# Optimization experiments

Measured on AMD Instinct MI355X. Metric: run time of the kernel, lower is better.

Reference implementation:

```python
import jax, jax.numpy as jnp
import numpy as np

N_NODES = 50000
N_EDGES = 800000
NFEAT = 96
NHID = 96
NCLASS = 40


def setup_inputs() -> dict:
    key = jax.random.key(0)
    ks = jax.random.split(key, 8)
    x = jax.random.normal(ks[0], (N_NODES, NFEAT), dtype=jnp.float32)
    edge_index = jax.random.randint(ks[1], (2, N_EDGES), 0, N_NODES, dtype=jnp.int64)
    def glorot(k, shape):
        fan_in = shape[1]
        bound = 1.0 / np.sqrt(fan_in)
        return jax.random.uniform(k, shape, jnp.float32, -bound, bound)
    return {
        'x': x,
        'edge_index': edge_index,
        'W1_l': glorot(ks[2], (NHID, NFEAT)),
        'b1_l': jnp.zeros((NHID,), jnp.float32),
        'W1_r': glorot(ks[3], (NHID, NFEAT)),
        'W2_l': glorot(ks[4], (NCLASS, NHID)),
        'b2_l': jnp.zeros((NCLASS,), jnp.float32),
        'W2_r': glorot(ks[5], (NCLASS, NHID)),
    }


def _sage_conv(x, src, dst, W_l, b_l, W_r):
    # gather neighbor features per edge, scatter-mean onto dst nodes
    msg = x[src]                                   # [E, F]
    agg = jax.ops.segment_sum(msg, dst, num_segments=N_NODES)   # [N, F]
    cnt = jax.ops.segment_sum(jnp.ones((src.shape[0],), x.dtype), dst,
                              num_segments=N_NODES)             # [N]
    agg = agg / jnp.maximum(cnt, 1.0)[:, None]
    # lin_l(agg) + lin_r(x)
    return agg @ W_l.T + b_l + x @ W_r.T


def reference(x, edge_index, W1_l, b1_l, W1_r, W2_l, b2_l, W2_r):
    src, dst = edge_index[0], edge_index[1]
    h = _sage_conv(x, src, dst, W1_l, b1_l, W1_r)
    h = jax.nn.relu(h)  # dropout is identity in eval mode
    h = _sage_conv(h, src, dst, W2_l, b2_l, W2_r)
    return jax.nn.log_softmax(h, axis=1)
```

## Files before the change

kernel.cpp:

```cpp
#include <hip/hip_runtime.h>
#include <math.h>

#define NCLASS 40
#define BSH    6
#define BSIZE  64
#define MAXB   1024
#define EPB    4096
#define LCOL   2048

typedef __attribute__((ext_vector_type(8))) short short8;
typedef __attribute__((ext_vector_type(4))) float float4v;

__device__ __forceinline__ unsigned short f2bf(float f) {
    union { float f; unsigned u; } v; v.f = f;
    unsigned r = v.u + 0x7fffu + ((v.u >> 16) & 1u);
    return (unsigned short)(r >> 16);
}
__device__ __forceinline__ float bf2f(unsigned int s) {
    union { unsigned u; float f; } v; v.u = s << 16; return v.f;
}

__global__ __launch_bounds__(256) void convhist_kernel(const int* __restrict__ ei,
                                                       const float4* __restrict__ x4,
                                                       const float* __restrict__ W1l,
                                                       const float* __restrict__ W1r,
                                                       const float* __restrict__ W2l,
                                                       const float* __restrict__ W2r,
                                                       int* __restrict__ histT,
                                                       unsigned short* __restrict__ axb,
                                                       unsigned short* __restrict__ wb1,
                                                       unsigned short* __restrict__ wb2,
                                                       int N, int E, int nbucket,
                                                       int nbin, int xblocks) {
    __shared__ int hcnt[MAXB];
    int tid = threadIdx.x;
    int blk = blockIdx.x;
    if (blk < nbin) {
        for (int t = tid; t < nbucket; t += 256) hcnt[t] = 0;
        __syncthreads();
        int e0 = blk * EPB;
        for (int it = 0; it < EPB / 256; ++it) {
            int e = e0 + it * 256 + tid;
            if (e < E) atomicAdd(&hcnt[ei[E + e] >> BSH], 1);
        }
        __syncthreads();
        for (int t = tid; t < nbucket; t += 256)
            histT[t * nbin + blk] = hcnt[t];
        return;
    }
    if (blk < nbin + xblocks) {
        int idx = (blk - nbin) * 256 + tid;
        if (idx >= N * 24) return;
        int n = idx / 24, q = idx - n * 24;
        float4 v = x4[idx];
        ushort4 o;
        o.x = f2bf(v.x); o.y = f2bf(v.y); o.z = f2bf(v.z); o.w = f2bf(v.w);
        *(ushort4*)(axb + (size_t)n * 192 + 96 + q * 4) = o;
        return;
    }
    int t = (blk - nbin - xblocks) * 256 + tid;
    const float* src;
    unsigned short* dst;
    if (t < 36 * 64) {
        int s = t >> 6, lane = t & 63;
        int kc = s / 6, jt = s - kc * 6;
        int j  = jt * 16 + (lane & 15);
        int k2 = kc * 32 + (lane >> 4) * 8;
        src = (k2 < 96) ? (W1l + j * 96 + k2) : (W1r + j * 96 + (k2 - 96));
        dst = wb1 + t * 8;
    } else if (t < 51 * 64) {
        int t2 = t - 36 * 64;
        int s = t2 >> 6, lane = t2 & 63;
        int kc = s / 5, jt = s - kc * 5;
        int j  = jt * 16 + (lane & 15);
        int k2 = kc * 32 + (lane >> 4) * 8;
        src = (j < 40) ? (W2l + j * 96 + k2) : (W2r + (j - 40) * 96 + k2);
        dst = wb2 + t2 * 8;
    } else return;
    ushort4 o0, o1;
    o0.x = f2bf(src[0]); o0.y = f2bf(src[1]); o0.z = f2bf(src[2]); o0.w = f2bf(src[3]);
    o1.x = f2bf(src[4]); o1.y = f2bf(src[5]); o1.z = f2bf(src[6]); o1.w = f2bf(src[7]);
    *(ushort4*)(dst)     = o0;
    *(ushort4*)(dst + 4) = o1;
}

__global__ __launch_bounds__(256) void bsum_kernel(int* __restrict__ histT,
                                                   int* __restrict__ gbh, int nbin) {
    __shared__ int s[256];
    int k = blockIdx.x, tid = threadIdx.x;
    int v = (tid < nbin) ? histT[k * nbin + tid] : 0;
    s[tid] = v;
    __syncthreads();
    for (int off = 1; off < 256; off <<= 1) {
        int o = (tid >= off) ? s[tid - off] : 0;
        __syncthreads();
        s[tid] += o;
        __syncthreads();
    }
    if (tid < nbin) histT[k * nbin + tid] = s[tid] - v;
    if (tid == 255) gbh[k] = s[255];
}

__global__ __launch_bounds__(256) void bscan_kernel(const int* __restrict__ gbh,
                                                    int* __restrict__ gbase,
                                                    int* __restrict__ rp,
                                                    int N, int E, int nbucket) {
    __shared__ int s[256];
    int tid  = threadIdx.x;
    int base = tid * 4;
    int w0 = (base     < nbucket) ? gbh[base]     : 0;
    int w1 = (base + 1 < nbucket) ? gbh[base + 1] : 0;
    int w2 = (base + 2 < nbucket) ? gbh[base + 2] : 0;
    int w3 = (base + 3 < nbucket) ? gbh[base + 3] : 0;
    int tsum = w0 + w1 + w2 + w3;
    s[tid] = tsum;
    __syncthreads();
    for (int off = 1; off < 256; off <<= 1) {
        int o = (tid >= off) ? s[tid - off] : 0;
        __syncthreads();
        s[tid] += o;
        __syncthreads();
    }
    int excl = s[tid] - tsum;
    if (base < nbucket) {
        gbase[base] = excl;
        if (base + 1 <= nbucket) gbase[base + 1] = excl + w0;
        if (base + 2 <= nbucket) gbase[base + 2] = excl + w0 + w1;
        if (base + 3 <= nbucket) gbase[base + 3] = excl + w0 + w1 + w2;
    }
    if (tid == 0) { gbase[nbucket] = E; rp[N] = E; }
}

__global__ __launch_bounds__(256) void bin_kernel(const int* __restrict__ ei,
                                                  const int* __restrict__ gbase,
                                                  const int* __restrict__ histT,
                                                  unsigned int* __restrict__ tmp,
                                                  int E, int nbucket, int nbin) {
    __shared__ int lcnt[MAXB];
    __shared__ int lbase[MAXB];
    int tid = threadIdx.x;
    for (int t = tid; t < nbucket; t += 256) {
        lbase[t] = gbase[t] + histT[t * nbin + blockIdx.x];
        lcnt[t]  = 0;
    }
    __syncthreads();
    int e0 = blockIdx.x * EPB;
    for (int it = 0; it < EPB / 256; ++it) {
        int e = e0 + it * 256 + tid;
        if (e < E) {
            int src = ei[e], dst = ei[E + e];
            int b   = dst >> BSH;
            int ofs = atomicAdd(&lcnt[b], 1);
            tmp[lbase[b] + ofs] = (unsigned)src | ((unsigned)(dst & (BSIZE - 1)) << 16);
        }
    }
}

__global__ __launch_bounds__(256) void csr_agg_kernel(const unsigned int* __restrict__ tmp,
                                                      const int* __restrict__ gbase,
                                                      int* __restrict__ rp,
                                                      unsigned short* __restrict__ col,
                                                      unsigned short* __restrict__ axb,
                                                      int N) {
    __shared__ int ncnt[BSIZE], nofs[BSIZE], sscan[BSIZE];
    __shared__ unsigned short lcol[LCOL];
    int b   = blockIdx.x;
    int tid = threadIdx.x;
    int s0 = gbase[b], s1 = gbase[b + 1];
    int cnt = s1 - s0;
    bool inl = (cnt <= LCOL);
    if (tid < BSIZE) ncnt[tid] = 0;
    __syncthreads();
    for (int i = s0 + tid; i < s1; i += 256)
        atomicAdd(&ncnt[tmp[i] >> 16], 1);
    __syncthreads();
    int v = (tid < BSIZE) ? ncnt[tid] : 0;
    if (tid < BSIZE) sscan[tid] = v;
    __syncthreads();
    for (int off = 1; off < BSIZE; off <<= 1) {
        int o = (tid < BSIZE && tid >= off) ? sscan[tid - off] : 0;
        __syncthreads();
        if (tid < BSIZE) sscan[tid] += o;
        __syncthreads();
    }
    if (tid < BSIZE) {
        nofs[tid] = sscan[tid] - v;
        int node = (b << BSH) + tid;
        if (node < N) rp[node] = s0 + nofs[tid];
        ncnt[tid] = 0;
    }
    __syncthreads();
    for (int i = s0 + tid; i < s1; i += 256) {
        unsigned int t2 = tmp[i];
        int d   = t2 >> 16;
        int ofs = atomicAdd(&ncnt[d], 1);
        int pos = nofs[d] + ofs;
        unsigned short sv = (unsigned short)(t2 & 0xffffu);
        col[s0 + pos] = sv;
        if (inl) lcol[pos] = sv;
    }
    __syncthreads();
    int nodebase = b << BSH;
    auto gather = [&](auto getc) {
        for (int item = tid; item < BSIZE * 12; item += 256) {
            int nl = item / 12;
            int q  = item - nl * 12;
            int ls  = nofs[nl];
            int deg = ncnt[nl];
            int le  = ls + deg;
            float a0=0.f,a1=0.f,a2=0.f,a3=0.f,a4=0.f,a5=0.f,a6=0.f,a7=0.f;
            int i = ls;
            for (; i + 7 < le; i += 8) {
                #pragma unroll
                for (int u = 0; u < 8; ++u) {
                    int c = getc(i + u);
                    uint4 w = *(const uint4*)(axb + (size_t)c * 192 + 96 + q * 8);
                    a0 += bf2f(w.x & 0xffffu); a1 += bf2f(w.x >> 16);
                    a2 += bf2f(w.y & 0xffffu); a3 += bf2f(w.y >> 16);
                    a4 += bf2f(w.z & 0xffffu); a5 += bf2f(w.z >> 16);
                    a6 += bf2f(w.w & 0xffffu); a7 += bf2f(w.w >> 16);
                }
            }
            for (; i < le; ++i) {
                int c = getc(i);
                uint4 w = *(const uint4*)(axb + (size_t)c * 192 + 96 + q * 8);
                a0 += bf2f(w.x & 0xffffu); a1 += bf2f(w.x >> 16);
                a2 += bf2f(w.y & 0xffffu); a3 += bf2f(w.y >> 16);
                a4 += bf2f(w.z & 0xffffu); a5 += bf2f(w.z >> 16);
                a6 += bf2f(w.w & 0xffffu); a7 += bf2f(w.w >> 16);
            }
            float inv = 1.0f / (float)(deg > 1 ? deg : 1);
            ushort4 o0, o1;
            o0.x = f2bf(a0 * inv); o0.y = f2bf(a1 * inv);
            o0.z = f2bf(a2 * inv); o0.w = f2bf(a3 * inv);
            o1.x = f2bf(a4 * inv); o1.y = f2bf(a5 * inv);
            o1.z = f2bf(a6 * inv); o1.w = f2bf(a7 * inv);
            *(ushort4*)(axb + (size_t)(nodebase + nl) * 192 + q * 8)     = o0;
            *(ushort4*)(axb + (size_t)(nodebase + nl) * 192 + q * 8 + 4) = o1;
        }
    };
    if (inl) gather([&](int i) { return (int)lcol[i]; });
    else     gather([&](int i) { return (int)col[s0 + i]; });
}

__global__ __launch_bounds__(256) void l1proj_kernel(const unsigned short* __restrict__ axb,
                                                     const unsigned short* __restrict__ wb1,
                                                     const float* __restrict__ b1,
                                                     const unsigned short* __restrict__ wb2,
                                                     const float* __restrict__ b2,
                                                     unsigned short* __restrict__ pl,
                                                     float* __restrict__ pr,
                                                     int N) {
    __shared__ unsigned short sh[128 * 104];
    int wave = threadIdx.x >> 6, lane = threadIdx.x & 63;
    int nbase = blockIdx.x * 128 + wave * 32;
    int lbase = wave * 32;
    int mrow = lane & 15, quad = lane >> 4;

    {
        float4v acc[2][6] = {};
        const short8* W = (const short8*)wb1;
        #pragma unroll
        for (int kc = 0; kc < 6; ++kc) {
            short8 a0 = *(const short8*)(axb + (size_t)(nbase + mrow)      * 192 + kc * 32 + quad * 8);
            short8 a1 = *(const short8*)(axb + (size_t)(nbase + 16 + mrow) * 192 + kc * 32 + quad * 8);
            #pragma unroll
            for (int jt = 0; jt < 6; ++jt) {
                short8 b = W[(kc * 6 + jt) * 64 + lane];
                acc[0][jt] = __builtin_amdgcn_mfma_f32_16x16x32_bf16(a0, b, acc[0][jt], 0, 0, 0);
                acc[1][jt] = __builtin_amdgcn_mfma_f32_16x16x32_bf16(a1, b, acc[1][jt], 0, 0, 0);
            }
        }
        #pragma unroll
        for (int jt = 0; jt < 6; ++jt) {
            int j = jt * 16 + mrow;
            float bj = b1[j];
            #pragma unroll
            for (int mt = 0; mt < 2; ++mt) {
                #pragma unroll
                for (int r = 0; r < 4; ++r) {
                    int nl = lbase + mt * 16 + quad * 4 + r;
                    sh[nl * 104 + j] = f2bf(fmaxf(acc[mt][jt][r] + bj, 0.f));
                }
            }
        }
    }
    __syncthreads();
    {
        float4v acc[2][5] = {};
        const short8* W = (const short8*)wb2;
        #pragma unroll
        for (int kc = 0; kc < 3; ++kc) {
            short8 a0 = *(const short8*)&sh[(lbase + mrow)      * 104 + kc * 32 + quad * 8];
            short8 a1 = *(const short8*)&sh[(lbase + 16 + mrow) * 104 + kc * 32 + quad * 8];
            #pragma unroll
            for (int jt = 0; jt < 5; ++jt) {
                short8 b = W[(kc * 5 + jt) * 64 + lane];
                acc[0][jt] = __builtin_amdgcn_mfma_f32_16x16x32_bf16(a0, b, acc[0][jt], 0, 0, 0);
                acc[1][jt] = __builtin_amdgcn_mfma_f32_16x16x32_bf16(a1, b, acc[1][jt], 0, 0, 0);
            }
        }
        #pragma unroll
        for (int jt = 0; jt < 5; ++jt) {
            int j = jt * 16 + mrow;
            float b2v = (j >= 40) ? b2[j - 40] : 0.f;
            #pragma unroll
            for (int mt = 0; mt < 2; ++mt) {
                #pragma unroll
                for (int r = 0; r < 4; ++r) {
                    int node = nbase + mt * 16 + quad * 4 + r;
                    if (node < N) {
                        float v = acc[mt][jt][r];
                        if (j < 40) pl[(size_t)node * 64 + j] = f2bf(v);
                        else        pr[(size_t)node * 40 + (j - 40)] = v + b2v;
                    }
                }
            }
        }
    }
}

__global__ __launch_bounds__(256) void final_kernel(const unsigned short* __restrict__ pl,
                                                    const float* __restrict__ pr,
                                                    const int* __restrict__ rp,
                                                    const unsigned short* __restrict__ col,
                                                    float* __restrict__ out, int N) {
    __shared__ float red[4][6][40];
    int wave = threadIdx.x >> 6;
    int lane = threadIdx.x & 63;
    int n = blockIdx.x * 4 + wave;
    if (n >= N) return;
    int s = rp[n], e = rp[n + 1];
    int g = lane / 10;
    int c = lane - g * 10;
    bool gok = (g < 6);
    float a0 = 0.f, a1 = 0.f, a2 = 0.f, a3 = 0.f;
    for (int base = s; base < e; base += 6) {
        int idx = base + g;
        if (gok && idx < e) {
            int cn = col[idx];
            uint2 u = *(const uint2*)(pl + (size_t)cn * 64 + c * 4);
            a0 += bf2f(u.x & 0xffffu); a1 += bf2f(u.x >> 16);
            a2 += bf2f(u.y & 0xffffu); a3 += bf2f(u.y >> 16);
        }
    }
    if (gok) {
        float4 t; t.x = a0; t.y = a1; t.z = a2; t.w = a3;
        *(float4*)&red[wave][g][c * 4] = t;
    }
    bool act = (lane < NCLASS);
    float v = -INFINITY;
    if (act) {
        float val = 0.f;
        #pragma unroll
        for (int gg = 0; gg < 6; ++gg) val += red[wave][gg][lane];
        int deg = e - s;
        float inv = 1.0f / (float)(deg > 1 ? deg : 1);
        v = val * inv + pr[(size_t)n * 40 + lane];
    }
    float m = v;
    #pragma unroll
    for (int off = 32; off >= 1; off >>= 1) m = fmaxf(m, __shfl_xor(m, off));
    float ex = act ? __expf(v - m) : 0.f;
    float ssum = ex;
    #pragma unroll
    for (int off = 32; off >= 1; off >>= 1) ssum += __shfl_xor(ssum, off);
    if (act) out[(size_t)n * 40 + lane] = v - m - __logf(ssum);
}

extern "C" void kernel_launch(void* const* d_in, const int* in_sizes, int n_in,
                              void* d_out, int out_size, void* d_ws, size_t ws_size,
                              hipStream_t stream) {
    const float* x   = (const float*)d_in[0];
    const int*   ei  = (const int*)  d_in[1];
    const float* W1l = (const float*)d_in[2];
    const float* b1  = (const float*)d_in[3];
    const float* W1r = (const float*)d_in[4];
    const float* W2l = (const float*)d_in[5];
    const float* b2  = (const float*)d_in[6];
    const float* W2r = (const float*)d_in[7];
    float* out = (float*)d_out;

    const int N = in_sizes[0] / 96;
    const int E = in_sizes[1] / 2;
    const int nbucket = (N + BSIZE - 1) >> BSH;
    const int nbin = (E + EPB - 1) / EPB;
    const int NB   = (N + 127) / 128;
    const int NP2  = NB * 128;
    const int xblocks = (N * 24 + 255) / 256;

    auto al = [](size_t v) { return (v + 255) & ~(size_t)255; };
    char* ws = (char*)d_ws;
    size_t o = 0;
    int* histT = (int*)(ws + o); o = al(o + (size_t)MAXB * 256 * 4);
    int* gbh   = (int*)(ws + o); o = al(o + (size_t)MAXB * 4);
    int* gbase = (int*)(ws + o); o = al(o + (size_t)(MAXB + 1) * 4);
    int* rp    = (int*)(ws + o); o = al(o + (size_t)(N + 1) * 4);
    unsigned int*   tmp = (unsigned int*)(ws + o);   o = al(o + (size_t)E * 4);
    unsigned short* col = (unsigned short*)(ws + o); o = al(o + (size_t)E * 2);
    unsigned short* axb = (unsigned short*)(ws + o); o = al(o + (size_t)NP2 * 192 * 2);
    unsigned short* wb1 = (unsigned short*)(ws + o); o = al(o + 36 * 64 * 8 * 2);
    unsigned short* wb2 = (unsigned short*)(ws + o); o = al(o + 15 * 64 * 8 * 2);
    unsigned short* pl  = (unsigned short*)(ws + o); o = al(o + (size_t)NP2 * 64 * 2);
    float*          pr  = (float*)(ws + o);          o = al(o + (size_t)N * 40 * 4);

    convhist_kernel<<<nbin + xblocks + 13, 256, 0, stream>>>(
        ei, (const float4*)x, W1l, W1r, W2l, W2r, histT, axb, wb1, wb2,
        N, E, nbucket, nbin, xblocks);
    bsum_kernel <<<nbucket, 256, 0, stream>>>(histT, gbh, nbin);
    bscan_kernel<<<1, 256, 0, stream>>>(gbh, gbase, rp, N, E, nbucket);
    bin_kernel  <<<nbin, 256, 0, stream>>>(ei, gbase, histT, tmp, E, nbucket, nbin);
    csr_agg_kernel<<<nbucket, 256, 0, stream>>>(tmp, gbase, rp, col, axb, N);
    l1proj_kernel<<<NB, 256, 0, stream>>>(axb, wb1, b1, wb2, b2, pl, pr, N);
    final_kernel<<<(N + 3) / 4, 256, 0, stream>>>(pl, pr, rp, col, out, N);
}
```

Measured before the change: 179.3 us.

## Split CSR finalize from aggregation into separate grid-wide gather kernel

Removes the fused gather from the per-bucket CSR kernel and launches a separate agg_kernel with one thread per node-chunk over all nodes, reading rp/col from global memory. Bucket size grows from 64 to 128 nodes, which halves the bucket count. The intent is to fix low occupancy and load imbalance in the gather, since the old kernel did it with only about 782 blocks and per-bucket degree skew. The cost is an extra kernel launch, a global round trip for col instead of LDS reuse, and larger buckets in the CSR kernels.

```diff
diff --git a/kernel.cpp b/kernel.cpp
--- a/kernel.cpp
+++ b/kernel.cpp
@@ -2,11 +2,10 @@
 #include <math.h>
 
 #define NCLASS 40
-#define BSH    6
-#define BSIZE  64
-#define MAXB   1024
+#define BSH    7
+#define BSIZE  128
+#define MAXB   512
 #define EPB    4096
-#define LCOL   2048
 
 typedef __attribute__((ext_vector_type(8))) short short8;
 typedef __attribute__((ext_vector_type(4))) float float4v;
@@ -156,19 +155,15 @@
     }
 }
 
-__global__ __launch_bounds__(256) void csr_agg_kernel(const unsigned int* __restrict__ tmp,
+__global__ __launch_bounds__(256) void csr_fin_kernel(const unsigned int* __restrict__ tmp,
                                                       const int* __restrict__ gbase,
                                                       int* __restrict__ rp,
                                                       unsigned short* __restrict__ col,
-                                                      unsigned short* __restrict__ axb,
                                                       int N) {
     __shared__ int ncnt[BSIZE], nofs[BSIZE], sscan[BSIZE];
-    __shared__ unsigned short lcol[LCOL];
     int b   = blockIdx.x;
     int tid = threadIdx.x;
     int s0 = gbase[b], s1 = gbase[b + 1];
-    int cnt = s1 - s0;
-    bool inl = (cnt <= LCOL);
     if (tid < BSIZE) ncnt[tid] = 0;
     __syncthreads();
     for (int i = s0 + tid; i < s1; i += 256)
@@ -194,53 +189,48 @@
         unsigned int t2 = tmp[i];
         int d   = t2 >> 16;
         int ofs = atomicAdd(&ncnt[d], 1);
-        int pos = nofs[d] + ofs;
-        unsigned short sv = (unsigned short)(t2 & 0xffffu);
-        col[s0 + pos] = sv;
-        if (inl) lcol[pos] = sv;
-    }
-    __syncthreads();
-    int nodebase = b << BSH;
-    auto gather = [&](auto getc) {
-        for (int item = tid; item < BSIZE * 12; item += 256) {
-            int nl = item / 12;
-            int q  = item - nl * 12;
-            int ls  = nofs[nl];
-            int deg = ncnt[nl];
-            int le  = ls + deg;
-            float a0=0.f,a1=0.f,a2=0.f,a3=0.f,a4=0.f,a5=0.f,a6=0.f,a7=0.f;
-            int i = ls;
-            for (; i + 7 < le; i += 8) {
-                #pragma unroll
-                for (int u = 0; u < 8; ++u) {
-                    int c = getc(i + u);
-                    uint4 w = *(const uint4*)(axb + (size_t)c * 192 + 96 + q * 8);
-                    a0 += bf2f(w.x & 0xffffu); a1 += bf2f(w.x >> 16);
-                    a2 += bf2f(w.y & 0xffffu); a3 += bf2f(w.y >> 16);
-                    a4 += bf2f(w.z & 0xffffu); a5 += bf2f(w.z >> 16);
-                    a6 += bf2f(w.w & 0xffffu); a7 += bf2f(w.w >> 16);
-                }
-            }
-            for (; i < le; ++i) {
-                int c = getc(i);
-                uint4 w = *(const uint4*)(axb + (size_t)c * 192 + 96 + q * 8);
-                a0 += bf2f(w.x & 0xffffu); a1 += bf2f(w.x >> 16);
-                a2 += bf2f(w.y & 0xffffu); a3 += bf2f(w.y >> 16);
-                a4 += bf2f(w.z & 0xffffu); a5 += bf2f(w.z >> 16);
-                a6 += bf2f(w.w & 0xffffu); a7 += bf2f(w.w >> 16);
-            }
-            float inv = 1.0f / (float)(deg > 1 ? deg : 1);
-            ushort4 o0, o1;
-            o0.x = f2bf(a0 * inv); o0.y = f2bf(a1 * inv);
-            o0.z = f2bf(a2 * inv); o0.w = f2bf(a3 * inv);
-            o1.x = f2bf(a4 * inv); o1.y = f2bf(a5 * inv);
-            o1.z = f2bf(a6 * inv); o1.w = f2bf(a7 * inv);
-            *(ushort4*)(axb + (size_t)(nodebase + nl) * 192 + q * 8)     = o0;
-            *(ushort4*)(axb + (size_t)(nodebase + nl) * 192 + q * 8 + 4) = o1;
-        }
-    };
-    if (inl) gather([&](int i) { return (int)lcol[i]; });
-    else     gather([&](int i) { return (int)col[s0 + i]; });
+        col[s0 + nofs[d] + ofs] = (unsigned short)(t2 & 0xffffu);
+    }
+}
+
+__global__ __launch_bounds__(256) void agg_kernel(const int* __restrict__ rp,
+                                                  const unsigned short* __restrict__ col,
+                                                  unsigned short* __restrict__ axb,
+                                                  int N) {
+    int idx = blockIdx.x * 256 + threadIdx.x;
+    if (idx >= N * 12) return;
+    int n = idx / 12, q = idx - n * 12;
+    int s = rp[n], e = rp[n + 1];
+    float a0=0.f,a1=0.f,a2=0.f,a3=0.f,a4=0.f,a5=0.f,a6=0.f,a7=0.f;
+    int i = s;
+    for (; i + 7 < e; i += 8) {
+        #pragma unroll
+        for (int u = 0; u < 8; ++u) {
+            int c = col[i + u];
+            uint4 w = *(const uint4*)(axb + (size_t)c * 192 + 96 + q * 8);
+            a0 += bf2f(w.x & 0xffffu); a1 += bf2f(w.x >> 16);
+            a2 += bf2f(w.y & 0xffffu); a3 += bf2f(w.y >> 16);
+            a4 += bf2f(w.z & 0xffffu); a5 += bf2f(w.z >> 16);
+            a6 += bf2f(w.w & 0xffffu); a7 += bf2f(w.w >> 16);
+        }
+    }
+    for (; i < e; ++i) {
+        int c = col[i];
+        uint4 w = *(const uint4*)(axb + (size_t)c * 192 + 96 + q * 8);
+        a0 += bf2f(w.x & 0xffffu); a1 += bf2f(w.x >> 16);
+        a2 += bf2f(w.y & 0xffffu); a3 += bf2f(w.y >> 16);
+        a4 += bf2f(w.z & 0xffffu); a5 += bf2f(w.z >> 16);
+        a6 += bf2f(w.w & 0xffffu); a7 += bf2f(w.w >> 16);
+    }
+    int deg = e - s;
+    float inv = 1.0f / (float)(deg > 1 ? deg : 1);
+    ushort4 o0, o1;
+    o0.x = f2bf(a0 * inv); o0.y = f2bf(a1 * inv);
+    o0.z = f2bf(a2 * inv); o0.w = f2bf(a3 * inv);
+    o1.x = f2bf(a4 * inv); o1.y = f2bf(a5 * inv);
+    o1.z = f2bf(a6 * inv); o1.w = f2bf(a7 * inv);
+    *(ushort4*)(axb + (size_t)n * 192 + q * 8)     = o0;
+    *(ushort4*)(axb + (size_t)n * 192 + q * 8 + 4) = o1;
 }
 
 __global__ __launch_bounds__(256) void l1proj_kernel(const unsigned short* __restrict__ axb,
@@ -410,7 +400,8 @@
     bsum_kernel <<<nbucket, 256, 0, stream>>>(histT, gbh, nbin);
     bscan_kernel<<<1, 256, 0, stream>>>(gbh, gbase, rp, N, E, nbucket);
     bin_kernel  <<<nbin, 256, 0, stream>>>(ei, gbase, histT, tmp, E, nbucket, nbin);
-    csr_agg_kernel<<<nbucket, 256, 0, stream>>>(tmp, gbase, rp, col, axb, N);
+    csr_fin_kernel<<<nbucket, 256, 0, stream>>>(tmp, gbase, rp, col, N);
+    agg_kernel<<<(N * 12 + 255) / 256, 256, 0, stream>>>(rp, col, axb, N);
     l1proj_kernel<<<NB, 256, 0, stream>>>(axb, wb1, b1, wb2, b2, pl, pr, N);
     final_kernel<<<(N + 3) / 4, 256, 0, stream>>>(pl, pr, rp, col, out, N);
 }
```

Result: no change. 182.4 us (+1.8%).
